# Kernel tuning notes

Measured on AMD Instinct MI355X. Metric: run time of the kernel, lower is better.

## Reference

```python
import jax, jax.numpy as jnp
import numpy as np

N_AXIS = 128      # n_x_axis == n_y_axis
N_TARGET = 8192


def setup_inputs() -> dict:
    key = jax.random.key(0)
    k1, k2 = jax.random.split(key, 2)
    # decoder output feature map: (4, n_y, n_x)
    feature_map = jax.random.normal(k1, (4, N_AXIS, N_AXIS), dtype=jnp.float32)
    # encoder grid: regular 2d grid in [-3, 3]^2, flattened (n_x*n_y, 2)
    ax = jnp.linspace(-3.0, 3.0, N_AXIS, dtype=jnp.float32)
    gx, gy = jnp.meshgrid(ax, ax, indexing='ij')
    grid = jnp.stack([gx, gy], axis=-1).reshape(N_AXIS * N_AXIS, 2)
    # target points in the same domain
    X_target = jax.random.uniform(k2, (N_TARGET, 2), dtype=jnp.float32,
                                  minval=-3.0, maxval=3.0)
    l_scale = jnp.float32(1.0)
    return {"feature_map": feature_map, "grid": grid,
            "X_target": X_target, "l_scale": l_scale}


def reference(feature_map, grid, X_target, l_scale):
    n_y, n_x = feature_map.shape[1], feature_map.shape[2]
    # Means_grid = FM[:2].permute(2,1,0).reshape(n_x*n_y, 2)
    means_grid = jnp.transpose(feature_map[:2], (2, 1, 0)).reshape(n_x * n_y, 2)
    # Sigmas_grid = softplus(FM[2:]), same permute/reshape
    sigmas_grid = jnp.transpose(jax.nn.softplus(feature_map[2:]), (2, 1, 0)).reshape(n_x * n_y, 2)
    # RBF kernel between targets and grid: K[t,g] = exp(-||xt-xg||^2 / (2 l^2))
    d2 = jnp.sum((X_target[:, None, :] - grid[None, :, :]) ** 2, axis=-1)  # [T, G]
    K = jnp.exp(-0.5 * d2 / (l_scale ** 2))
    denom = jnp.sum(K, axis=1, keepdims=True)  # normalized (Nadaraya-Watson)
    means_target = (K @ means_grid) / denom    # [T, 2]
    sigmas_target = (K @ sigmas_grid) / denom  # [T, 2]
    return means_target, sigmas_target
```

## Files before the change

kernel.cpp:

```cpp
#include <hip/hip_runtime.h>
#include <hip/hip_bf16.h>
#include <math.h>


#define NA      128
#define TT      16
#define THREADS 512

typedef __attribute__((ext_vector_type(8))) short short8;
typedef __attribute__((ext_vector_type(4))) float f32x4;

__device__ __forceinline__ short f2bf(float x) {
    __hip_bfloat16 h = __float2bfloat16(x);
    return *reinterpret_cast<short*>(&h);
}

__global__ __launch_bounds__(256)
void pack_pre(const float* __restrict__ fm, short* __restrict__ bfB)
{
    const int idx = blockIdx.x * 256 + threadIdx.x;
    const int c  = idx >> 12;
    const int k  = (idx >> 5) & 127;
    const int i0 = (idx & 31) * 4;

    float4 v = *reinterpret_cast<const float4*>(fm + c * NA * NA + k * NA + i0);
    if (c >= 2) {
        v.x = (v.x > 15.0f) ? v.x : log1pf(__expf(v.x));
        v.y = (v.y > 15.0f) ? v.y : log1pf(__expf(v.y));
        v.z = (v.z > 15.0f) ? v.z : log1pf(__expf(v.z));
        v.w = (v.w > 15.0f) ? v.w : log1pf(__expf(v.w));
    }
    const int s = k >> 5;
    const int e = k & 7;
    const int Lk = ((k >> 3) & 3) * 16;
    const float vv[4] = {v.x, v.y, v.z, v.w};
#pragma unroll
    for (int d = 0; d < 4; ++d) {
        const int i = i0 + d;
        const int n = i >> 4;
        const int L = Lk + (i & 15);
        bfB[(((c * 8 + n) * 4 + s) * 64 + L) * 8 + e] = f2bf(vv[d]);
    }
}

__global__ __launch_bounds__(THREADS)
void cnp_mfma(const short* __restrict__ bfB,
              const float* __restrict__ grid,
              const float* __restrict__ xt,
              const float* __restrict__ lsp,
              float* __restrict__ out,
              int n_target)
{
    __shared__ __attribute__((aligned(16))) float Kx[TT * NA];
    __shared__ __attribute__((aligned(16))) float Ky32[TT * NA];
    __shared__ __attribute__((aligned(16))) short kyA[4 * 64 * 8];
    __shared__ float psx[TT], psy[TT];
    __shared__ float red[4][2][TT];

    const int tid  = threadIdx.x;
    const int wid  = tid >> 6;
    const int c    = wid & 3;
    const int nh   = wid >> 2;
    const int lane = tid & 63;
    const int t0   = blockIdx.x * TT;

    const short8* bbase = reinterpret_cast<const short8*>(bfB)
                        + c * 2048 + nh * 4 * 256 + lane;
    const short8 b00 = bbase[0],         b01 = bbase[64],
                 b02 = bbase[128],       b03 = bbase[192];
    const short8 b10 = bbase[256],       b11 = bbase[256 + 64],
                 b12 = bbase[256 + 128], b13 = bbase[256 + 192];
    const short8 b20 = bbase[512],       b21 = bbase[512 + 64],
                 b22 = bbase[512 + 128], b23 = bbase[512 + 192];
    const short8 b30 = bbase[768],       b31 = bbase[768 + 64],
                 b32 = bbase[768 + 128], b33 = bbase[768 + 192];

    const float l      = lsp[0];
    const float inv2l2 = 0.5f / (l * l);

#pragma unroll
    for (int s = 0; s < 4; ++s) {
        const int k = s * THREADS + tid;
        const int t = k >> 7;
        const int j = k & 127;
        int tg = t0 + t; if (tg >= n_target) tg = n_target - 1;
        const float ax = grid[j * 2 + 1];
        const float dx = xt[tg * 2 + 0] - ax;
        const float dy = xt[tg * 2 + 1] - ax;
        const float kxv = __expf(-dx * dx * inv2l2);
        const float kyv = __expf(-dy * dy * inv2l2);
        Kx[t * NA + j]   = kxv;
        Ky32[t * NA + j] = kyv;
        const int ss = j >> 5, g = (j & 31) >> 3, e = j & 7;
        kyA[((ss * 64) + g * 16 + (t & 15)) * 8 + e] = f2bf(kyv);
    }
    __syncthreads();

    {
        const int grp  = tid >> 4;
        const int l16  = tid & 15;
        const int t    = grp >> 1;
        const int axis = grp & 1;
        const float* kb = axis ? Ky32 : Kx;
        const float4 q0 = *reinterpret_cast<const float4*>(&kb[t * NA + l16 * 8]);
        const float4 q1 = *reinterpret_cast<const float4*>(&kb[t * NA + l16 * 8 + 4]);
        float u = ((q0.x + q0.y) + (q0.z + q0.w)) + ((q1.x + q1.y) + (q1.z + q1.w));
        u += __shfl_xor(u, 1); u += __shfl_xor(u, 2);
        u += __shfl_xor(u, 4); u += __shfl_xor(u, 8);
        if (l16 == 0) { if (axis) psy[t] = u; else psx[t] = u; }
    }

    const short8* kap = reinterpret_cast<const short8*>(kyA);
    const short8 a0 = kap[0 * 64 + lane];
    const short8 a1 = kap[1 * 64 + lane];
    const short8 a2 = kap[2 * 64 + lane];
    const short8 a3 = kap[3 * 64 + lane];

    const int icol = lane & 15;
    const int tb   = (lane >> 4) * 4;
    f32x4 p = {0.f, 0.f, 0.f, 0.f};

#define NTILE(NN, B0, B1, B2, B3)                                              \
    {                                                                          \
        f32x4 acc = {0.f, 0.f, 0.f, 0.f};                                      \
        acc = __builtin_amdgcn_mfma_f32_16x16x32_bf16(a0, B0, acc, 0, 0, 0);   \
        acc = __builtin_amdgcn_mfma_f32_16x16x32_bf16(a1, B1, acc, 0, 0, 0);   \
        acc = __builtin_amdgcn_mfma_f32_16x16x32_bf16(a2, B2, acc, 0, 0, 0);   \
        acc = __builtin_amdgcn_mfma_f32_16x16x32_bf16(a3, B3, acc, 0, 0, 0);   \
        const int i = (nh * 4 + (NN)) * 16 + icol;                             \
        p.x = fmaf(Kx[(tb + 0) * NA + i], acc.x, p.x);                         \
        p.y = fmaf(Kx[(tb + 1) * NA + i], acc.y, p.y);                         \
        p.z = fmaf(Kx[(tb + 2) * NA + i], acc.z, p.z);                         \
        p.w = fmaf(Kx[(tb + 3) * NA + i], acc.w, p.w);                         \
    }
    NTILE(0, b00, b01, b02, b03)
    NTILE(1, b10, b11, b12, b13)
    NTILE(2, b20, b21, b22, b23)
    NTILE(3, b30, b31, b32, b33)
#undef NTILE

#pragma unroll
    for (int st = 1; st <= 8; st <<= 1) {
        p.x += __shfl_xor(p.x, st);
        p.y += __shfl_xor(p.y, st);
        p.z += __shfl_xor(p.z, st);
        p.w += __shfl_xor(p.w, st);
    }
    if ((lane & 15) == 0) {
        red[c][nh][tb + 0] = p.x;
        red[c][nh][tb + 1] = p.y;
        red[c][nh][tb + 2] = p.z;
        red[c][nh][tb + 3] = p.w;
    }
    __syncthreads();

    if (tid < 4 * TT) {
        const int t  = tid & (TT - 1);
        const int cc = tid >> 4;
        const int tg = t0 + t;
        if (tg < n_target) {
            const float numer = red[cc][0][t] + red[cc][1][t];
            const float val = numer / (psx[t] * psy[t]);
            if (cc < 2) out[tg * 2 + cc] = val;
            else        out[n_target * 2 + tg * 2 + (cc - 2)] = val;
        }
    }
}

extern "C" void kernel_launch(void* const* d_in, const int* in_sizes, int n_in,
                              void* d_out, int out_size, void* d_ws, size_t ws_size,
                              hipStream_t stream) {
    const float* fm   = (const float*)d_in[0];
    const float* grid = (const float*)d_in[1];
    const float* xt   = (const float*)d_in[2];
    const float* lsp  = (const float*)d_in[3];
    float* out = (float*)d_out;
    short* bfB = (short*)d_ws;

    const int n_target = in_sizes[2] / 2;

    hipLaunchKernelGGL(pack_pre, dim3(64), dim3(256), 0, stream, fm, bfB);

    const int blocks = (n_target + TT - 1) / TT;
    hipLaunchKernelGGL(cnp_mfma, dim3(blocks), dim3(THREADS), 0, stream,
                       bfB, grid, xt, lsp, out, n_target);
}
```

Measured before the change: 15.14 us.

## Move RBF factor computation into prep kernel and stage via global workspace

Per-target Kx/Ky factor evaluation, bf16 A-operand packing and row sums move from the MFMA kernel into the prep kernel, which gets extra blocks next to the feature-map packing blocks. The main kernel then loads precomputed A fragments, Kx rows and sums from global memory instead of computing exps and running an LDS reduction. This shortens the main kernel and drops two LDS arrays and a reduction phase. In exchange it writes and re-reads about 4 MB of Kx data plus the packed A tiles through global memory.

```diff
diff --git a/kernel.cpp b/kernel.cpp
--- a/kernel.cpp
+++ b/kernel.cpp
@@ -16,45 +16,86 @@
 }
 
 __global__ __launch_bounds__(256)
-void pack_pre(const float* __restrict__ fm, short* __restrict__ bfB)
+void prep(const float* __restrict__ fm, const float* __restrict__ grid,
+          const float* __restrict__ xt, const float* __restrict__ lsp,
+          short* __restrict__ bfB, short* __restrict__ aT,
+          float* __restrict__ KxT, float* __restrict__ SxT,
+          float* __restrict__ SyT, int n_target)
 {
-    const int idx = blockIdx.x * 256 + threadIdx.x;
-    const int c  = idx >> 12;
-    const int k  = (idx >> 5) & 127;
-    const int i0 = (idx & 31) * 4;
-
-    float4 v = *reinterpret_cast<const float4*>(fm + c * NA * NA + k * NA + i0);
-    if (c >= 2) {
-        v.x = (v.x > 15.0f) ? v.x : log1pf(__expf(v.x));
-        v.y = (v.y > 15.0f) ? v.y : log1pf(__expf(v.y));
-        v.z = (v.z > 15.0f) ? v.z : log1pf(__expf(v.z));
-        v.w = (v.w > 15.0f) ? v.w : log1pf(__expf(v.w));
-    }
-    const int s = k >> 5;
-    const int e = k & 7;
-    const int Lk = ((k >> 3) & 3) * 16;
-    const float vv[4] = {v.x, v.y, v.z, v.w};
+    const int tid = threadIdx.x;
+
+    if (blockIdx.x < 64) {
+        const int idx = blockIdx.x * 256 + tid;
+        const int c  = idx >> 12;
+        const int k  = (idx >> 5) & 127;
+        const int i0 = (idx & 31) * 4;
+        float4 v = *reinterpret_cast<const float4*>(fm + c * NA * NA + k * NA + i0);
+        if (c >= 2) {
+            v.x = (v.x > 15.0f) ? v.x : log1pf(__expf(v.x));
+            v.y = (v.y > 15.0f) ? v.y : log1pf(__expf(v.y));
+            v.z = (v.z > 15.0f) ? v.z : log1pf(__expf(v.z));
+            v.w = (v.w > 15.0f) ? v.w : log1pf(__expf(v.w));
+        }
+        const int s  = k >> 5;
+        const int e  = k & 7;
+        const int Lk = ((k >> 3) & 3) * 16;
+        const float vv[4] = {v.x, v.y, v.z, v.w};
 #pragma unroll
-    for (int d = 0; d < 4; ++d) {
-        const int i = i0 + d;
-        const int n = i >> 4;
-        const int L = Lk + (i & 15);
-        bfB[(((c * 8 + n) * 4 + s) * 64 + L) * 8 + e] = f2bf(vv[d]);
-    }
+        for (int d = 0; d < 4; ++d) {
+            const int i = i0 + d;
+            const int n = i >> 4;
+            const int L = Lk + (i & 15);
+            bfB[(((c * 8 + n) * 4 + s) * 64 + L) * 8 + e] = f2bf(vv[d]);
+        }
+        return;
+    }
+
+    const int t0   = (blockIdx.x - 64) * 32;
+    const int tloc = tid >> 3;
+    const int jg   = tid & 7;
+    const int t    = t0 + tloc;
+    int tg = t; if (tg >= n_target) tg = n_target - 1;
+    const float x0 = xt[tg * 2 + 0];
+    const float x1 = xt[tg * 2 + 1];
+    const float l      = lsp[0];
+    const float inv2l2 = 0.5f / (l * l);
+    const int bA   = t >> 4;
+    const int mloc = t & 15;
+
+    float sx = 0.f, sy = 0.f;
+#pragma unroll
+    for (int q = 0; q < 4; ++q) {
+        float kx0, kx1, kx2, kx3;
+#define KPT(D, KX)                                                             \
+        {                                                                      \
+            const int j = jg * 16 + q * 4 + (D);                               \
+            const float ax = grid[j * 2 + 1];         \
+            const float dx = x0 - ax, dy = x1 - ax;                            \
+            KX = __expf(-dx * dx * inv2l2);                                    \
+            const float ky = __expf(-dy * dy * inv2l2);                        \
+            sx += KX; sy += ky;                                                \
+            aT[((bA * 4 + (j >> 5)) * 64 + ((j & 31) >> 3) * 16 + mloc) * 8    \
+               + (j & 7)] = f2bf(ky);                                          \
+        }
+        KPT(0, kx0) KPT(1, kx1) KPT(2, kx2) KPT(3, kx3)
+#undef KPT
+        const float4 o = {kx0, kx1, kx2, kx3};
+        *reinterpret_cast<float4*>(&KxT[t * NA + jg * 16 + q * 4]) = o;
+    }
+    sx += __shfl_xor(sx, 1); sy += __shfl_xor(sy, 1);
+    sx += __shfl_xor(sx, 2); sy += __shfl_xor(sy, 2);
+    sx += __shfl_xor(sx, 4); sy += __shfl_xor(sy, 4);
+    if (jg == 0) { SxT[t] = sx; SyT[t] = sy; }
 }
 
 __global__ __launch_bounds__(THREADS)
 void cnp_mfma(const short* __restrict__ bfB,
-              const float* __restrict__ grid,
-              const float* __restrict__ xt,
-              const float* __restrict__ lsp,
-              float* __restrict__ out,
-              int n_target)
+              const short* __restrict__ aT,
+              const float* __restrict__ KxT,
+              const float* __restrict__ SxT, const float* __restrict__ SyT,
+              float* __restrict__ out, int n_target)
 {
     __shared__ __attribute__((aligned(16))) float Kx[TT * NA];
-    __shared__ __attribute__((aligned(16))) float Ky32[TT * NA];
-    __shared__ __attribute__((aligned(16))) short kyA[4 * 64 * 8];
-    __shared__ float psx[TT], psy[TT];
     __shared__ float red[4][2][TT];
 
     const int tid  = threadIdx.x;
@@ -75,46 +116,15 @@
     const short8 b30 = bbase[768],       b31 = bbase[768 + 64],
                  b32 = bbase[768 + 128], b33 = bbase[768 + 192];
 
-    const float l      = lsp[0];
-    const float inv2l2 = 0.5f / (l * l);
-
-#pragma unroll
-    for (int s = 0; s < 4; ++s) {
-        const int k = s * THREADS + tid;
-        const int t = k >> 7;
-        const int j = k & 127;
-        int tg = t0 + t; if (tg >= n_target) tg = n_target - 1;
-        const float ax = grid[j * 2 + 1];
-        const float dx = xt[tg * 2 + 0] - ax;
-        const float dy = xt[tg * 2 + 1] - ax;
-        const float kxv = __expf(-dx * dx * inv2l2);
-        const float kyv = __expf(-dy * dy * inv2l2);
-        Kx[t * NA + j]   = kxv;
-        Ky32[t * NA + j] = kyv;
-        const int ss = j >> 5, g = (j & 31) >> 3, e = j & 7;
-        kyA[((ss * 64) + g * 16 + (t & 15)) * 8 + e] = f2bf(kyv);
+    const short8* abase = reinterpret_cast<const short8*>(aT)
+                        + blockIdx.x * 256 + lane;
+    const short8 a0 = abase[0], a1 = abase[64], a2 = abase[128], a3 = abase[192];
+
+    {
+        const float4 kq = *reinterpret_cast<const float4*>(&KxT[t0 * NA + tid * 4]);
+        *reinterpret_cast<float4*>(&Kx[tid * 4]) = kq;
     }
     __syncthreads();
-
-    {
-        const int grp  = tid >> 4;
-        const int l16  = tid & 15;
-        const int t    = grp >> 1;
-        const int axis = grp & 1;
-        const float* kb = axis ? Ky32 : Kx;
-        const float4 q0 = *reinterpret_cast<const float4*>(&kb[t * NA + l16 * 8]);
-        const float4 q1 = *reinterpret_cast<const float4*>(&kb[t * NA + l16 * 8 + 4]);
-        float u = ((q0.x + q0.y) + (q0.z + q0.w)) + ((q1.x + q1.y) + (q1.z + q1.w));
-        u += __shfl_xor(u, 1); u += __shfl_xor(u, 2);
-        u += __shfl_xor(u, 4); u += __shfl_xor(u, 8);
-        if (l16 == 0) { if (axis) psy[t] = u; else psx[t] = u; }
-    }
-
-    const short8* kap = reinterpret_cast<const short8*>(kyA);
-    const short8 a0 = kap[0 * 64 + lane];
-    const short8 a1 = kap[1 * 64 + lane];
-    const short8 a2 = kap[2 * 64 + lane];
-    const short8 a3 = kap[3 * 64 + lane];
 
     const int icol = lane & 15;
     const int tb   = (lane >> 4) * 4;
@@ -160,7 +170,7 @@
         const int tg = t0 + t;
         if (tg < n_target) {
             const float numer = red[cc][0][t] + red[cc][1][t];
-            const float val = numer / (psx[t] * psy[t]);
+            const float val = numer / (SxT[tg] * SyT[tg]);
             if (cc < 2) out[tg * 2 + cc] = val;
             else        out[n_target * 2 + tg * 2 + (cc - 2)] = val;
         }
@@ -175,13 +185,21 @@
     const float* xt   = (const float*)d_in[2];
     const float* lsp  = (const float*)d_in[3];
     float* out = (float*)d_out;
-    short* bfB = (short*)d_ws;
 
     const int n_target = in_sizes[2] / 2;
-
-    hipLaunchKernelGGL(pack_pre, dim3(64), dim3(256), 0, stream, fm, bfB);
-
-    const int blocks = (n_target + TT - 1) / TT;
-    hipLaunchKernelGGL(cnp_mfma, dim3(blocks), dim3(THREADS), 0, stream,
-                       bfB, grid, xt, lsp, out, n_target);
-}
+    const int nb32 = (n_target + 31) / 32;
+    const int nb16 = (n_target + 15) / 16;
+    const int NTp  = nb32 * 32;
+
+    char* w = (char*)d_ws;
+    short* bfB = (short*)w;                      w += (size_t)65536 * 2;
+    short* aT  = (short*)w;                      w += (size_t)nb16 * 2048 * 2;
+    float* KxT = (float*)w;                      w += (size_t)NTp * NA * 4;
+    float* SxT = (float*)w;                      w += (size_t)NTp * 4;
+    float* SyT = (float*)w;
+
+    hipLaunchKernelGGL(prep, dim3(64 + nb32), dim3(256), 0, stream,
+                       fm, grid, xt, lsp, bfB, aT, KxT, SxT, SyT, n_target);
+    hipLaunchKernelGGL(cnp_mfma, dim3(nb16), dim3(THREADS), 0, stream,
+                       bfB, aT, KxT, SxT, SyT, out, n_target);
+}
```

New measurement: 18.16 us. 1.2x slower.

## Compute RBF factors directly in registers, removing shared-memory staging and a barrier

Applied to the files above, without the earlier changes.

Each wave now computes its own bf16 Ky A-fragments and the fp32 Kx factors straight into registers from the grid and target coordinates. This replaces the shared-memory Kx/Ky tables, the first __syncthreads, and the LDS reads that fed the MFMA and epilogue. Row sums for the denominators come from in-register shuffles: Sy is computed redundantly per wave, and Sx is split across the two n-halves and summed at the end. The cost is more redundant exp evaluations and global loads per wave, in exchange for less LDS traffic and one fewer block-wide barrier. Sy is now summed from fp32 values before bf16 rounding, the same as before.

```diff
diff --git a/kernel.cpp b/kernel.cpp
--- a/kernel.cpp
+++ b/kernel.cpp
@@ -30,8 +30,8 @@
         v.z = (v.z > 15.0f) ? v.z : log1pf(__expf(v.z));
         v.w = (v.w > 15.0f) ? v.w : log1pf(__expf(v.w));
     }
-    const int s = k >> 5;
-    const int e = k & 7;
+    const int s  = k >> 5;
+    const int e  = k & 7;
     const int Lk = ((k >> 3) & 3) * 16;
     const float vv[4] = {v.x, v.y, v.z, v.w};
 #pragma unroll
@@ -51,21 +51,21 @@
               float* __restrict__ out,
               int n_target)
 {
-    __shared__ __attribute__((aligned(16))) float Kx[TT * NA];
-    __shared__ __attribute__((aligned(16))) float Ky32[TT * NA];
-    __shared__ __attribute__((aligned(16))) short kyA[4 * 64 * 8];
-    __shared__ float psx[TT], psy[TT];
     __shared__ float red[4][2][TT];
+    __shared__ float psx[TT][2];
+    __shared__ float psy[TT];
 
     const int tid  = threadIdx.x;
     const int wid  = tid >> 6;
     const int c    = wid & 3;
     const int nh   = wid >> 2;
     const int lane = tid & 63;
+    const int g    = lane >> 4;
+    const int m    = lane & 15;
     const int t0   = blockIdx.x * TT;
 
     const short8* bbase = reinterpret_cast<const short8*>(bfB)
-                        + c * 2048 + nh * 4 * 256 + lane;
+                        + c * 2048 + nh * 1024 + lane;
     const short8 b00 = bbase[0],         b01 = bbase[64],
                  b02 = bbase[128],       b03 = bbase[192];
     const short8 b10 = bbase[256],       b11 = bbase[256 + 64],
@@ -78,65 +78,65 @@
     const float l      = lsp[0];
     const float inv2l2 = 0.5f / (l * l);
 
-#pragma unroll
-    for (int s = 0; s < 4; ++s) {
-        const int k = s * THREADS + tid;
-        const int t = k >> 7;
-        const int j = k & 127;
-        int tg = t0 + t; if (tg >= n_target) tg = n_target - 1;
-        const float ax = grid[j * 2 + 1];
-        const float dx = xt[tg * 2 + 0] - ax;
-        const float dy = xt[tg * 2 + 1] - ax;
-        const float kxv = __expf(-dx * dx * inv2l2);
-        const float kyv = __expf(-dy * dy * inv2l2);
-        Kx[t * NA + j]   = kxv;
-        Ky32[t * NA + j] = kyv;
-        const int ss = j >> 5, g = (j & 31) >> 3, e = j & 7;
-        kyA[((ss * 64) + g * 16 + (t & 15)) * 8 + e] = f2bf(kyv);
-    }
-    __syncthreads();
-
-    {
-        const int grp  = tid >> 4;
-        const int l16  = tid & 15;
-        const int t    = grp >> 1;
-        const int axis = grp & 1;
-        const float* kb = axis ? Ky32 : Kx;
-        const float4 q0 = *reinterpret_cast<const float4*>(&kb[t * NA + l16 * 8]);
-        const float4 q1 = *reinterpret_cast<const float4*>(&kb[t * NA + l16 * 8 + 4]);
-        float u = ((q0.x + q0.y) + (q0.z + q0.w)) + ((q1.x + q1.y) + (q1.z + q1.w));
-        u += __shfl_xor(u, 1); u += __shfl_xor(u, 2);
-        u += __shfl_xor(u, 4); u += __shfl_xor(u, 8);
-        if (l16 == 0) { if (axis) psy[t] = u; else psx[t] = u; }
-    }
-
-    const short8* kap = reinterpret_cast<const short8*>(kyA);
-    const short8 a0 = kap[0 * 64 + lane];
-    const short8 a1 = kap[1 * 64 + lane];
-    const short8 a2 = kap[2 * 64 + lane];
-    const short8 a3 = kap[3 * 64 + lane];
-
-    const int icol = lane & 15;
-    const int tb   = (lane >> 4) * 4;
+    int tgm = t0 + m; if (tgm >= n_target) tgm = n_target - 1;
+    const float ty = xt[tgm * 2 + 1];
+    float syp = 0.0f;
+    short8 a0, a1, a2, a3;
+#define AFRAG(AS, S)                                                           \
+    {                                                                          \
+        short8 av;                                                             \
+        _Pragma("unroll")                                                      \
+        for (int e = 0; e < 8; ++e) {                                          \
+            const int j = (S) * 32 + g * 8 + e;                                \
+            const float axv = grid[j * 2 + 1];                                 \
+            const float d   = ty - axv;                                        \
+            const float kv  = __expf(-d * d * inv2l2);                         \
+            syp += kv;                                                         \
+            av[e] = f2bf(kv);                                                  \
+        }                                                                      \
+        AS = av;                                                               \
+    }
+    AFRAG(a0, 0) AFRAG(a1, 1) AFRAG(a2, 2) AFRAG(a3, 3)
+#undef AFRAG
+    syp += __shfl_xor(syp, 16);
+    syp += __shfl_xor(syp, 32);
+    if (wid == 0 && lane < 16) psy[lane] = syp;
+
+    const int tb = g * 4;
+    int tr0 = t0 + tb + 0; if (tr0 >= n_target) tr0 = n_target - 1;
+    int tr1 = t0 + tb + 1; if (tr1 >= n_target) tr1 = n_target - 1;
+    int tr2 = t0 + tb + 2; if (tr2 >= n_target) tr2 = n_target - 1;
+    int tr3 = t0 + tb + 3; if (tr3 >= n_target) tr3 = n_target - 1;
+    const float tx0 = xt[tr0 * 2], tx1 = xt[tr1 * 2],
+                tx2 = xt[tr2 * 2], tx3 = xt[tr3 * 2];
+    const float axi0 = grid[(((nh * 4 + 0) * 16 + m) * 2) + 1];
+    const float axi1 = grid[(((nh * 4 + 1) * 16 + m) * 2) + 1];
+    const float axi2 = grid[(((nh * 4 + 2) * 16 + m) * 2) + 1];
+    const float axi3 = grid[(((nh * 4 + 3) * 16 + m) * 2) + 1];
+#define KXE(TX, AX) __expf(-((TX) - (AX)) * ((TX) - (AX)) * inv2l2)
+    f32x4 kx0 = {KXE(tx0, axi0), KXE(tx1, axi0), KXE(tx2, axi0), KXE(tx3, axi0)};
+    f32x4 kx1 = {KXE(tx0, axi1), KXE(tx1, axi1), KXE(tx2, axi1), KXE(tx3, axi1)};
+    f32x4 kx2 = {KXE(tx0, axi2), KXE(tx1, axi2), KXE(tx2, axi2), KXE(tx3, axi2)};
+    f32x4 kx3 = {KXE(tx0, axi3), KXE(tx1, axi3), KXE(tx2, axi3), KXE(tx3, axi3)};
+#undef KXE
+
     f32x4 p = {0.f, 0.f, 0.f, 0.f};
-
-#define NTILE(NN, B0, B1, B2, B3)                                              \
+#define NTILE(KX, B0, B1, B2, B3)                                              \
     {                                                                          \
         f32x4 acc = {0.f, 0.f, 0.f, 0.f};                                      \
         acc = __builtin_amdgcn_mfma_f32_16x16x32_bf16(a0, B0, acc, 0, 0, 0);   \
         acc = __builtin_amdgcn_mfma_f32_16x16x32_bf16(a1, B1, acc, 0, 0, 0);   \
         acc = __builtin_amdgcn_mfma_f32_16x16x32_bf16(a2, B2, acc, 0, 0, 0);   \
         acc = __builtin_amdgcn_mfma_f32_16x16x32_bf16(a3, B3, acc, 0, 0, 0);   \
-        const int i = (nh * 4 + (NN)) * 16 + icol;                             \
-        p.x = fmaf(Kx[(tb + 0) * NA + i], acc.x, p.x);                         \
-        p.y = fmaf(Kx[(tb + 1) * NA + i], acc.y, p.y);                         \
-        p.z = fmaf(Kx[(tb + 2) * NA + i], acc.z, p.z);                         \
-        p.w = fmaf(Kx[(tb + 3) * NA + i], acc.w, p.w);                         \
-    }
-    NTILE(0, b00, b01, b02, b03)
-    NTILE(1, b10, b11, b12, b13)
-    NTILE(2, b20, b21, b22, b23)
-    NTILE(3, b30, b31, b32, b33)
+        p.x = fmaf(KX.x, acc.x, p.x);                                          \
+        p.y = fmaf(KX.y, acc.y, p.y);                                          \
+        p.z = fmaf(KX.z, acc.z, p.z);                                          \
+        p.w = fmaf(KX.w, acc.w, p.w);                                          \
+    }
+    NTILE(kx0, b00, b01, b02, b03)
+    NTILE(kx1, b10, b11, b12, b13)
+    NTILE(kx2, b20, b21, b22, b23)
+    NTILE(kx3, b30, b31, b32, b33)
 #undef NTILE
 
 #pragma unroll
@@ -146,11 +146,32 @@
         p.z += __shfl_xor(p.z, st);
         p.w += __shfl_xor(p.w, st);
     }
-    if ((lane & 15) == 0) {
+    if (m == 0) {
         red[c][nh][tb + 0] = p.x;
         red[c][nh][tb + 1] = p.y;
         red[c][nh][tb + 2] = p.z;
         red[c][nh][tb + 3] = p.w;
+    }
+
+    if (c == 0) {
+        f32x4 q;
+        q.x = (kx0.x + kx1.x) + (kx2.x + kx3.x);
+        q.y = (kx0.y + kx1.y) + (kx2.y + kx3.y);
+        q.z = (kx0.z + kx1.z) + (kx2.z + kx3.z);
+        q.w = (kx0.w + kx1.w) + (kx2.w + kx3.w);
+#pragma unroll
+        for (int st = 1; st <= 8; st <<= 1) {
+            q.x += __shfl_xor(q.x, st);
+            q.y += __shfl_xor(q.y, st);
+            q.z += __shfl_xor(q.z, st);
+            q.w += __shfl_xor(q.w, st);
+        }
+        if (m == 0) {
+            psx[tb + 0][nh] = q.x;
+            psx[tb + 1][nh] = q.y;
+            psx[tb + 2][nh] = q.z;
+            psx[tb + 3][nh] = q.w;
+        }
     }
     __syncthreads();
 
@@ -160,7 +181,8 @@
         const int tg = t0 + t;
         if (tg < n_target) {
             const float numer = red[cc][0][t] + red[cc][1][t];
-            const float val = numer / (psx[t] * psy[t]);
+            const float Sx = psx[t][0] + psx[t][1];
+            const float val = numer / (Sx * psy[t]);
             if (cc < 2) out[tg * 2 + cc] = val;
             else        out[n_target * 2 + tg * 2 + (cc - 2)] = val;
         }
```

New measurement: 16.03 us. +5.9%, slower.
